# Optimization experiments

Hardware: AMD Instinct MI355X
Metric: run time of the kernel (lower is better)

Reference implementation:

```python
import jax, jax.numpy as jnp
import numpy as np

D_MODEL = 1024
HEAD_SIZE = 64
BLOCK_SIZE = 2048
B, T = 4, 2048


def setup_inputs() -> dict:
    key = jax.random.key(0)
    ks = jax.random.split(key, 7)
    s = 1.0 / np.sqrt(D_MODEL)
    x = jax.random.normal(ks[0], (B, T, D_MODEL), dtype=jnp.float32)
    Wq = jax.random.uniform(ks[1], (D_MODEL, HEAD_SIZE), jnp.float32, -s, s)
    bq = jax.random.uniform(ks[2], (HEAD_SIZE,), jnp.float32, -s, s)
    Wk = jax.random.uniform(ks[3], (D_MODEL, HEAD_SIZE), jnp.float32, -s, s)
    bk = jax.random.uniform(ks[4], (HEAD_SIZE,), jnp.float32, -s, s)
    Wv = jax.random.uniform(ks[5], (D_MODEL, HEAD_SIZE), jnp.float32, -s, s)
    return {"x": x, "Wq": Wq, "bq": bq, "Wk": Wk, "bk": bk, "Wv": Wv, "mask": 1}


def reference(x, Wq, bq, Wk, bk, Wv, mask):
    # x: [B, T, C]; single attention head, dropout is identity (eval/p=0)
    Tlen = x.shape[1]
    q = x @ Wq + bq              # [B, T, hs]
    k = x @ Wk + bk              # [B, T, hs]
    v = x @ Wv                   # [B, T, hs] (no bias)
    hs = k.shape[-1]
    # Faithful to source: weights = QK^T / hs**(-0.5)  ==  QK^T * sqrt(hs)
    w = jnp.einsum('btd,bsd->bts', q, k) * jnp.sqrt(jnp.asarray(hs, x.dtype))
    if mask:
        causal = jnp.tril(jnp.ones((Tlen, Tlen), dtype=bool))
        w = jnp.where(causal, w, jnp.asarray(-jnp.inf, w.dtype))
    w = jax.nn.softmax(w, axis=-1)
    out = jnp.einsum('bts,bsd->btd', w, v)  # [B, T, hs]
    return out
```

## Files before the change

kernel.cpp:

```cpp
#include <hip/hip_runtime.h>
#include <hip/hip_bf16.h>

#define D_MODEL 1024
#define HS 64
#define T_LEN 2048
#define JCH 256
#define NCH 8

typedef __attribute__((ext_vector_type(8))) short bf16x8;
typedef __attribute__((ext_vector_type(4))) float f32x4;

__device__ inline void split8(const float* v, int4& hi, int4& lo) {
    union { unsigned short u[8]; int4 v4; } uh, ul;
    #pragma unroll
    for (int i = 0; i < 8; ++i) {
        const unsigned int b = __float_as_uint(v[i]);
        const unsigned short h = (unsigned short)(b >> 16);
        const float r = v[i] - __uint_as_float((unsigned int)h << 16);
        uh.u[i] = h;
        ul.u[i] = (unsigned short)(__float_as_uint(r) >> 16);
    }
    hi = uh.v4; lo = ul.v4;
}

__device__ inline void split8b(const float* v, bf16x8& hi, bf16x8& lo) {
    union { unsigned short u[8]; bf16x8 v8; } uh, ul;
    #pragma unroll
    for (int i = 0; i < 8; ++i) {
        const unsigned int b = __float_as_uint(v[i]);
        const unsigned short h = (unsigned short)(b >> 16);
        const float r = v[i] - __uint_as_float((unsigned int)h << 16);
        uh.u[i] = h;
        ul.u[i] = (unsigned short)(__float_as_uint(r) >> 16);
    }
    hi = uh.v8; lo = ul.v8;
}

__device__ inline unsigned short f2bf_rne(float f) {
    const unsigned int b = __float_as_uint(f);
    return (unsigned short)((b + 0x7FFFu + ((b >> 16) & 1u)) >> 16);
}
__device__ inline float bf2f(unsigned short h) {
    return __uint_as_float((unsigned int)h << 16);
}

__device__ inline void async_copy16(const short* g, short* l) {
    __builtin_amdgcn_global_load_lds(
        (const __attribute__((address_space(1))) void*)g,
        (__attribute__((address_space(3))) void*)l, 16, 0, 0);
}

__global__ __launch_bounds__(256) void prep_kernel(
    const float* __restrict__ Wq, const float* __restrict__ Wk,
    const float* __restrict__ Wv,
    short* __restrict__ wh, short* __restrict__ wl)
{
    __shared__ float tile[64][69];
    const int tid = threadIdx.x;
    const int wb  = blockIdx.x;
    const int kb  = wb & 15;
    const int m   = wb >> 4;
    const float* W = (m == 0) ? Wq : (m == 1) ? Wk : Wv;
    #pragma unroll
    for (int it = 0; it < 4; ++it) {
        const int idx = tid + 256 * it;
        const int kr = idx >> 4, c4 = idx & 15;
        *(float4*)&tile[kr][4 * c4] =
            *(const float4*)(W + (size_t)(kb * 64 + kr) * HS + 4 * c4);
    }
    __syncthreads();
    #pragma unroll
    for (int i = 0; i < 2; ++i) {
        const int s    = tid + 256 * i;
        const int ntl  = s >> 7;
        const int kcl  = (s >> 6) & 1;
        const int lane = s & 63;
        const int n    = ntl * 16 + (lane & 15);
        const int krel = kcl * 32 + (lane >> 4) * 8;
        float v[8];
        #pragma unroll
        for (int e = 0; e < 8; ++e) v[e] = tile[krel + e][n];
        int4 hi, lo;
        split8(v, hi, lo);
        const size_t off =
            ((size_t)((m * 4 + ntl) * 32 + kb * 2 + kcl) * 64 + lane) * 8;
        *(int4*)(wh + off) = hi;
        *(int4*)(wl + off) = lo;
    }
}

__global__ __launch_bounds__(512, 2) void qkv_kernel(
    const float* __restrict__ x,
    const short* __restrict__ wh, const short* __restrict__ wl,
    const float* __restrict__ bq, const float* __restrict__ bk,
    short* __restrict__ qfh, short* __restrict__ qfl,
    short* __restrict__ kfh, short* __restrict__ kfl, short* __restrict__ vf)
{
    const int tid  = threadIdx.x;
    const int wv   = tid >> 6;
    const int lane = tid & 63;
    const int mt   = wv & 1;
    const int nt0  = (wv >> 1) * 3;
    const int r0   = blockIdx.x * 32;

    const float* xrow = x + (size_t)(r0 + mt * 16 + (lane & 15)) * D_MODEL
                          + (lane >> 4) * 8;

    f32x4 acc[3];
    #pragma unroll
    for (int j = 0; j < 3; ++j) acc[j] = (f32x4)(0.f);

    #pragma unroll
    for (int t = 0; t < 16; ++t) {
        const float* xc = xrow + t * 64;
        float v0[8], v1[8];
        *(float4*)&v0[0] = *(const float4*)(xc);
        *(float4*)&v0[4] = *(const float4*)(xc + 4);
        *(float4*)&v1[0] = *(const float4*)(xc + 32);
        *(float4*)&v1[4] = *(const float4*)(xc + 36);

        bf16x8 bh[2][3], bl[2][3];
        #pragma unroll
        for (int kcl = 0; kcl < 2; ++kcl)
            #pragma unroll
            for (int j = 0; j < 3; ++j) {
                const size_t off =
                    ((size_t)((nt0 + j) * 32 + t * 2 + kcl)) * 512 + lane * 8;
                bh[kcl][j] = *(const bf16x8*)&wh[off];
                bl[kcl][j] = *(const bf16x8*)&wl[off];
            }

        bf16x8 a0h, a0l, a1h, a1l;
        split8b(v0, a0h, a0l);
        split8b(v1, a1h, a1l);

        #pragma unroll
        for (int j = 0; j < 3; ++j) {
            acc[j] = __builtin_amdgcn_mfma_f32_16x16x32_bf16(a0h, bh[0][j], acc[j], 0, 0, 0);
            acc[j] = __builtin_amdgcn_mfma_f32_16x16x32_bf16(a0h, bl[0][j], acc[j], 0, 0, 0);
            acc[j] = __builtin_amdgcn_mfma_f32_16x16x32_bf16(a0l, bh[0][j], acc[j], 0, 0, 0);
        }
        #pragma unroll
        for (int j = 0; j < 3; ++j) {
            acc[j] = __builtin_amdgcn_mfma_f32_16x16x32_bf16(a1h, bh[1][j], acc[j], 0, 0, 0);
            acc[j] = __builtin_amdgcn_mfma_f32_16x16x32_bf16(a1h, bl[1][j], acc[j], 0, 0, 0);
            acc[j] = __builtin_amdgcn_mfma_f32_16x16x32_bf16(a1l, bh[1][j], acc[j], 0, 0, 0);
        }
    }

    const int quad = lane >> 4;
    const int l15  = lane & 15;
    const int rowb = r0 + mt * 16 + quad * 4;
    #pragma unroll
    for (int j = 0; j < 3; ++j) {
        const f32x4 a = acc[j];
        const int c = (nt0 + j) * 16 + l15;
        if (c < 128) {
            const int cc    = (c < 64) ? c : (c - 64);
            const float bias = (c < 64) ? bq[cc] : bk[cc];
            short* dsth = (c < 64) ? qfh : kfh;
            short* dstl = (c < 64) ? qfl : kfl;
            const int tile16 = rowb >> 4;
            const int kc2   = cc >> 5;
            const int quadd = (cc & 31) >> 3;
            const int e     = cc & 7;
            #pragma unroll
            for (int r = 0; r < 4; ++r) {
                const float val = a[r] + bias;
                const unsigned int b = __float_as_uint(val);
                const unsigned short h = (unsigned short)(b >> 16);
                const float res = val - __uint_as_float((unsigned int)h << 16);
                const unsigned short l16 = (unsigned short)(__float_as_uint(res) >> 16);
                const int laned = ((rowb + r) & 15) | (quadd << 4);
                const size_t off = ((size_t)((tile16 * 2 + kc2) * 64 + laned)) * 8 + e;
                dsth[off] = (short)h;
                dstl[off] = (short)l16;
            }
        } else {
            const int cv    = c - 128;
            const int vb    = rowb >> 6;
            const int jc2   = (rowb & 63) >> 5;
            const int quadd = (rowb & 31) >> 3;
            const int gg    = jc2 * 4 + (cv >> 4);
            const int laned = (cv & 15) | (quadd << 4);
            const size_t base = ((size_t)((vb * 8 + gg) * 64 + laned)) * 8 + (rowb & 7);
            short4 pk;
            pk.x = (short)f2bf_rne(a[0]);
            pk.y = (short)f2bf_rne(a[1]);
            pk.z = (short)f2bf_rne(a[2]);
            pk.w = (short)f2bf_rne(a[3]);
            *(short4*)(vf + base) = pk;
        }
    }
}

__global__ __launch_bounds__(256) void attn_kernel(
    const short* __restrict__ qfh, const short* __restrict__ qfl,
    const short* __restrict__ kfh, const short* __restrict__ kfl,
    const short* __restrict__ vf, const int* __restrict__ maskp,
    float* __restrict__ part_O, float* __restrict__ part_ml, int BT)
{
    __shared__ __align__(16) short Kh[4096], Kl[4096];
    __shared__ __align__(16) short Vt[4096];
    __shared__ __align__(16) short Pl[4][16 * 72];

    const int tile  = blockIdx.x;
    const int chunk = blockIdx.y;
    const int r0 = tile * 64;
    const int tb = r0 / T_LEN;
    const int t0 = r0 - tb * T_LEN;
    const int mask = (*maskp != 0);
    const int n_max = mask ? (t0 + 64) : T_LEN;
    const int j0 = chunk * JCH;
    if (j0 >= n_max) return;
    const int hi_j = min(j0 + JCH, n_max);
    const int njt = (hi_j - j0 + 63) >> 6;

    const int tid  = threadIdx.x;
    const int w    = tid >> 6;
    const int lane = tid & 63;
    const int quad = lane >> 4;
    const int l15  = lane & 15;
    const int rw0  = t0 + 16 * w;
    const int rowa = r0 + 16 * w + quad * 4;

    bf16x8 qh[2], ql[2];
    {
        const size_t qt = (size_t)(r0 >> 4) + w;
        #pragma unroll
        for (int kc = 0; kc < 2; ++kc) {
            qh[kc] = *(const bf16x8*)&qfh[((qt * 2 + kc) * 64 + lane) * 8];
            ql[kc] = *(const bf16x8*)&qfl[((qt * 2 + kc) * 64 + lane) * 8];
        }
    }

    f32x4 oacc[4];
    #pragma unroll
    for (int nt = 0; nt < 4; ++nt) oacc[nt] = (f32x4)(0.f);
    float m_r[4] = {-INFINITY, -INFINITY, -INFINITY, -INFINITY};
    float l_r[4] = {0.f, 0.f, 0.f, 0.f};

    for (int jt = 0; jt < njt; ++jt) {
        const int jbase = j0 + jt * 64;
        __syncthreads();
        {
            const size_t kt0 = (size_t)(tb * 128) + (jbase >> 4);
            const size_t vb  = (size_t)(tb * 32) + (jbase >> 6);
            #pragma unroll
            for (int ii = 0; ii < 6; ++ii) {
                const int g = w * 6 + ii;
                if (g < 8) {
                    const short* src = kfh + ((kt0 + (g >> 1)) * 2 + (g & 1)) * 512;
                    async_copy16(src + lane * 8, &Kh[g * 512]);
                } else if (g < 16) {
                    const int gg = g - 8;
                    const short* src = kfl + ((kt0 + (gg >> 1)) * 2 + (gg & 1)) * 512;
                    async_copy16(src + lane * 8, &Kl[gg * 512]);
                } else {
                    const int gg = g - 16;
                    const short* src = vf + (vb * 8 + gg) * 512;
                    async_copy16(src + lane * 8, &Vt[gg * 512]);
                }
            }
        }
        __syncthreads();

        const bool active = (!mask) || (jbase <= rw0 + 15);
        if (active) {
            f32x4 sacc[4];
            #pragma unroll
            for (int jsub = 0; jsub < 4; ++jsub) {
                f32x4 s = (f32x4)(0.f);
                #pragma unroll
                for (int kc = 0; kc < 2; ++kc) {
                    const bf16x8 kh = *(const bf16x8*)&Kh[((jsub * 2 + kc) * 64 + lane) * 8];
                    const bf16x8 kl = *(const bf16x8*)&Kl[((jsub * 2 + kc) * 64 + lane) * 8];
                    s = __builtin_amdgcn_mfma_f32_16x16x32_bf16(qh[kc], kh, s, 0, 0, 0);
                    s = __builtin_amdgcn_mfma_f32_16x16x32_bf16(qh[kc], kl, s, 0, 0, 0);
                    s = __builtin_amdgcn_mfma_f32_16x16x32_bf16(ql[kc], kh, s, 0, 0, 0);
                }
                sacc[jsub] = s;
            }
            float sval[4][4], rmax[4];
            #pragma unroll
            for (int r = 0; r < 4; ++r) rmax[r] = -INFINITY;
            #pragma unroll
            for (int jsub = 0; jsub < 4; ++jsub) {
                const int jg = jbase + jsub * 16 + l15;
                #pragma unroll
                for (int r = 0; r < 4; ++r) {
                    const int tg = rw0 + quad * 4 + r;
                    const float vv = (mask && (jg > tg)) ? -INFINITY : 8.0f * sacc[jsub][r];
                    sval[jsub][r] = vv;
                    rmax[r] = fmaxf(rmax[r], vv);
                }
            }
            #pragma unroll
            for (int d = 1; d < 16; d <<= 1)
                #pragma unroll
                for (int r = 0; r < 4; ++r)
                    rmax[r] = fmaxf(rmax[r], __shfl_xor(rmax[r], d));
            float alpha[4], msafe[4];
            #pragma unroll
            for (int r = 0; r < 4; ++r) {
                const float mn = fmaxf(m_r[r], rmax[r]);
                msafe[r] = (mn == -INFINITY) ? 0.f : mn;
                alpha[r] = __expf(m_r[r] - msafe[r]);
                m_r[r] = mn;
            }
            short* Pw = &Pl[w][0];
            float rsum[4] = {0.f, 0.f, 0.f, 0.f};
            #pragma unroll
            for (int jsub = 0; jsub < 4; ++jsub) {
                #pragma unroll
                for (int r = 0; r < 4; ++r) {
                    const float e = __expf(sval[jsub][r] - msafe[r]);
                    const unsigned short eb = f2bf_rne(e);
                    Pw[(quad * 4 + r) * 72 + jsub * 16 + l15] = (short)eb;
                    rsum[r] += bf2f(eb);
                }
            }
            #pragma unroll
            for (int d = 1; d < 16; d <<= 1)
                #pragma unroll
                for (int r = 0; r < 4; ++r)
                    rsum[r] += __shfl_xor(rsum[r], d);
            #pragma unroll
            for (int r = 0; r < 4; ++r)
                l_r[r] = l_r[r] * alpha[r] + rsum[r];
            #pragma unroll
            for (int nt = 0; nt < 4; ++nt)
                #pragma unroll
                for (int r = 0; r < 4; ++r)
                    oacc[nt][r] *= alpha[r];
            bf16x8 pf[2];
            #pragma unroll
            for (int jc = 0; jc < 2; ++jc)
                pf[jc] = *(const bf16x8*)&Pw[l15 * 72 + jc * 32 + quad * 8];
            #pragma unroll
            for (int nt = 0; nt < 4; ++nt) {
                #pragma unroll
                for (int jc = 0; jc < 2; ++jc) {
                    const bf16x8 vfr = *(const bf16x8*)&Vt[((jc * 4 + nt) * 64 + lane) * 8];
                    oacc[nt] = __builtin_amdgcn_mfma_f32_16x16x32_bf16(pf[jc], vfr, oacc[nt], 0, 0, 0);
                }
            }
        }
    }

    #pragma unroll
    for (int nt = 0; nt < 4; ++nt)
        #pragma unroll
        for (int r = 0; r < 4; ++r)
            part_O[((size_t)(rowa + r) * NCH + chunk) * HS + nt * 16 + l15] = oacc[nt][r];
    if (l15 == 0) {
        #pragma unroll
        for (int r = 0; r < 4; ++r) {
            float2 ml;
            ml.x = m_r[r];
            ml.y = l_r[r];
            *(float2*)(part_ml + ((size_t)(rowa + r) * NCH + chunk) * 2) = ml;
        }
    }
}

__global__ __launch_bounds__(256) void combine_kernel(
    const float* __restrict__ part_O, const float* __restrict__ part_ml,
    const int* __restrict__ maskp, float* __restrict__ out)
{
    const int f = blockIdx.x * 256 + threadIdx.x;
    const int row = f >> 4;
    const int d4 = (f & 15) * 4;
    const int t = row & (T_LEN - 1);
    const int mask = (*maskp != 0);
    const int n = mask ? (t + 1) : T_LEN;
    const int nc = (n + JCH - 1) / JCH;

    const float2* mlp = (const float2*)(part_ml + (size_t)row * NCH * 2);
    float M = -INFINITY;
    for (int c = 0; c < nc; ++c) M = fmaxf(M, mlp[c].x);
    float L = 0.f;
    float Ox = 0.f, Oy = 0.f, Oz = 0.f, Ow = 0.f;
    for (int c = 0; c < nc; ++c) {
        const float2 ml = mlp[c];
        const float w = __expf(ml.x - M);
        L += ml.y * w;
        const float4 p = *(const float4*)(part_O + ((size_t)row * NCH + c) * HS + d4);
        Ox = fmaf(p.x, w, Ox);
        Oy = fmaf(p.y, w, Oy);
        Oz = fmaf(p.z, w, Oz);
        Ow = fmaf(p.w, w, Ow);
    }
    float4 res;
    res.x = Ox / L;
    res.y = Oy / L;
    res.z = Oz / L;
    res.w = Ow / L;
    *(float4*)(out + (size_t)row * HS + d4) = res;
}

extern "C" void kernel_launch(void* const* d_in, const int* in_sizes, int n_in,
                              void* d_out, int out_size, void* d_ws, size_t ws_size,
                              hipStream_t stream) {
    const float* x  = (const float*)d_in[0];
    const float* Wq = (const float*)d_in[1];
    const float* bq = (const float*)d_in[2];
    const float* Wk = (const float*)d_in[3];
    const float* bk = (const float*)d_in[4];
    const float* Wv = (const float*)d_in[5];
    const int* maskp = (const int*)d_in[6];

    const int BT = in_sizes[0] / D_MODEL;

    float* pO  = (float*)d_ws;
    float* pml = pO + (size_t)BT * NCH * HS;
    short* wh  = (short*)(pml + (size_t)BT * NCH * 2);
    short* wl  = wh + (size_t)192 * D_MODEL;
    short* qfh = wl + (size_t)192 * D_MODEL;
    short* qfl = qfh + (size_t)BT * HS;
    short* kfh = qfl + (size_t)BT * HS;
    short* kfl = kfh + (size_t)BT * HS;
    short* vf  = kfl + (size_t)BT * HS;

    prep_kernel<<<48, 256, 0, stream>>>(Wq, Wk, Wv, wh, wl);
    qkv_kernel<<<BT / 32, 512, 0, stream>>>(x, wh, wl, bq, bk,
                                            qfh, qfl, kfh, kfl, vf);
    dim3 agrid(BT / 64, NCH);
    attn_kernel<<<agrid, 256, 0, stream>>>(qfh, qfl, kfh, kfl, vf, maskp,
                                           pO, pml, BT);
    combine_kernel<<<(BT * 16) / 256, 256, 0, stream>>>(pO, pml, maskp, (float*)d_out);
}
```

Before: 142.9 us.

## Split QKV projection into finer per-matrix blocks with XCD-aware block ordering

Result: slower. 165.1 us (+15.5%).

```diff
diff --git a/kernel.cpp b/kernel.cpp
--- a/kernel.cpp
+++ b/kernel.cpp
@@ -21,19 +21,6 @@
         ul.u[i] = (unsigned short)(__float_as_uint(r) >> 16);
     }
     hi = uh.v4; lo = ul.v4;
-}
-
-__device__ inline void split8b(const float* v, bf16x8& hi, bf16x8& lo) {
-    union { unsigned short u[8]; bf16x8 v8; } uh, ul;
-    #pragma unroll
-    for (int i = 0; i < 8; ++i) {
-        const unsigned int b = __float_as_uint(v[i]);
-        const unsigned short h = (unsigned short)(b >> 16);
-        const float r = v[i] - __uint_as_float((unsigned int)h << 16);
-        uh.u[i] = h;
-        ul.u[i] = (unsigned short)(__float_as_uint(r) >> 16);
-    }
-    hi = uh.v8; lo = ul.v8;
 }
 
 __device__ inline unsigned short f2bf_rne(float f) {
@@ -89,108 +76,108 @@
     }
 }
 
-__global__ __launch_bounds__(512, 2) void qkv_kernel(
+__device__ __forceinline__ void split_frag(const float4& p, const float4& q,
+                                           bf16x8& hi, bf16x8& lo) {
+    const float v[8] = {p.x, p.y, p.z, p.w, q.x, q.y, q.z, q.w};
+    #pragma unroll
+    for (int i = 0; i < 8; ++i) {
+        const unsigned int b = __float_as_uint(v[i]);
+        const unsigned short h = (unsigned short)(b >> 16);
+        const float r = v[i] - __uint_as_float((unsigned int)h << 16);
+        hi[i] = (short)h;
+        lo[i] = (short)(__float_as_uint(r) >> 16);
+    }
+}
+
+__global__ __launch_bounds__(256, 4) void qkv_kernel(
     const float* __restrict__ x,
     const short* __restrict__ wh, const short* __restrict__ wl,
     const float* __restrict__ bq, const float* __restrict__ bk,
     short* __restrict__ qfh, short* __restrict__ qfl,
-    short* __restrict__ kfh, short* __restrict__ kfl, short* __restrict__ vf)
+    short* __restrict__ kfh, short* __restrict__ kfl, short* __restrict__ vf,
+    int BT)
 {
     const int tid  = threadIdx.x;
-    const int wv   = tid >> 6;
+    const int w    = tid >> 6;
     const int lane = tid & 63;
-    const int mt   = wv & 1;
-    const int nt0  = (wv >> 1) * 3;
-    const int r0   = blockIdx.x * 32;
-
-    const float* xrow = x + (size_t)(r0 + mt * 16 + (lane & 15)) * D_MODEL
+
+    const int perx = ((BT >> 4) * 3) >> 3;
+    const int work = ((int)blockIdx.x >> 3) + ((int)blockIdx.x & 7) * perx;
+    const int g    = work / 3;
+    const int m    = work - g * 3;
+    const int r0   = g * 16;
+    const int gnt  = m * 4 + w;
+
+    const float* xrow = x + (size_t)(r0 + (lane & 15)) * D_MODEL
                           + (lane >> 4) * 8;
 
-    f32x4 acc[3];
-    #pragma unroll
-    for (int j = 0; j < 3; ++j) acc[j] = (f32x4)(0.f);
+    f32x4 acc = (f32x4)(0.f);
 
     #pragma unroll
     for (int t = 0; t < 16; ++t) {
+        const size_t ob0 = ((size_t)(gnt * 32 + t * 2 + 0)) * 512 + lane * 8;
+        const size_t ob1 = ((size_t)(gnt * 32 + t * 2 + 1)) * 512 + lane * 8;
+        const bf16x8 bh0 = *(const bf16x8*)&wh[ob0];
+        const bf16x8 bl0 = *(const bf16x8*)&wl[ob0];
+        const bf16x8 bh1 = *(const bf16x8*)&wh[ob1];
+        const bf16x8 bl1 = *(const bf16x8*)&wl[ob1];
+
         const float* xc = xrow + t * 64;
-        float v0[8], v1[8];
-        *(float4*)&v0[0] = *(const float4*)(xc);
-        *(float4*)&v0[4] = *(const float4*)(xc + 4);
-        *(float4*)&v1[0] = *(const float4*)(xc + 32);
-        *(float4*)&v1[4] = *(const float4*)(xc + 36);
-
-        bf16x8 bh[2][3], bl[2][3];
-        #pragma unroll
-        for (int kcl = 0; kcl < 2; ++kcl)
-            #pragma unroll
-            for (int j = 0; j < 3; ++j) {
-                const size_t off =
-                    ((size_t)((nt0 + j) * 32 + t * 2 + kcl)) * 512 + lane * 8;
-                bh[kcl][j] = *(const bf16x8*)&wh[off];
-                bl[kcl][j] = *(const bf16x8*)&wl[off];
-            }
+        const float4 xa = *(const float4*)(xc);
+        const float4 xb = *(const float4*)(xc + 4);
+        const float4 xm = *(const float4*)(xc + 32);
+        const float4 xd = *(const float4*)(xc + 36);
 
         bf16x8 a0h, a0l, a1h, a1l;
-        split8b(v0, a0h, a0l);
-        split8b(v1, a1h, a1l);
-
-        #pragma unroll
-        for (int j = 0; j < 3; ++j) {
-            acc[j] = __builtin_amdgcn_mfma_f32_16x16x32_bf16(a0h, bh[0][j], acc[j], 0, 0, 0);
-            acc[j] = __builtin_amdgcn_mfma_f32_16x16x32_bf16(a0h, bl[0][j], acc[j], 0, 0, 0);
-            acc[j] = __builtin_amdgcn_mfma_f32_16x16x32_bf16(a0l, bh[0][j], acc[j], 0, 0, 0);
-        }
-        #pragma unroll
-        for (int j = 0; j < 3; ++j) {
-            acc[j] = __builtin_amdgcn_mfma_f32_16x16x32_bf16(a1h, bh[1][j], acc[j], 0, 0, 0);
-            acc[j] = __builtin_amdgcn_mfma_f32_16x16x32_bf16(a1h, bl[1][j], acc[j], 0, 0, 0);
-            acc[j] = __builtin_amdgcn_mfma_f32_16x16x32_bf16(a1l, bh[1][j], acc[j], 0, 0, 0);
-        }
+        split_frag(xa, xb, a0h, a0l);
+        split_frag(xm, xd, a1h, a1l);
+
+        acc = __builtin_amdgcn_mfma_f32_16x16x32_bf16(a0h, bh0, acc, 0, 0, 0);
+        acc = __builtin_amdgcn_mfma_f32_16x16x32_bf16(a0h, bl0, acc, 0, 0, 0);
+        acc = __builtin_amdgcn_mfma_f32_16x16x32_bf16(a0l, bh0, acc, 0, 0, 0);
+        acc = __builtin_amdgcn_mfma_f32_16x16x32_bf16(a1h, bh1, acc, 0, 0, 0);
+        acc = __builtin_amdgcn_mfma_f32_16x16x32_bf16(a1h, bl1, acc, 0, 0, 0);
+        acc = __builtin_amdgcn_mfma_f32_16x16x32_bf16(a1l, bh1, acc, 0, 0, 0);
     }
 
     const int quad = lane >> 4;
     const int l15  = lane & 15;
-    const int rowb = r0 + mt * 16 + quad * 4;
-    #pragma unroll
-    for (int j = 0; j < 3; ++j) {
-        const f32x4 a = acc[j];
-        const int c = (nt0 + j) * 16 + l15;
-        if (c < 128) {
-            const int cc    = (c < 64) ? c : (c - 64);
-            const float bias = (c < 64) ? bq[cc] : bk[cc];
-            short* dsth = (c < 64) ? qfh : kfh;
-            short* dstl = (c < 64) ? qfl : kfl;
-            const int tile16 = rowb >> 4;
-            const int kc2   = cc >> 5;
-            const int quadd = (cc & 31) >> 3;
-            const int e     = cc & 7;
-            #pragma unroll
-            for (int r = 0; r < 4; ++r) {
-                const float val = a[r] + bias;
-                const unsigned int b = __float_as_uint(val);
-                const unsigned short h = (unsigned short)(b >> 16);
-                const float res = val - __uint_as_float((unsigned int)h << 16);
-                const unsigned short l16 = (unsigned short)(__float_as_uint(res) >> 16);
-                const int laned = ((rowb + r) & 15) | (quadd << 4);
-                const size_t off = ((size_t)((tile16 * 2 + kc2) * 64 + laned)) * 8 + e;
-                dsth[off] = (short)h;
-                dstl[off] = (short)l16;
-            }
-        } else {
-            const int cv    = c - 128;
-            const int vb    = rowb >> 6;
-            const int jc2   = (rowb & 63) >> 5;
-            const int quadd = (rowb & 31) >> 3;
-            const int gg    = jc2 * 4 + (cv >> 4);
-            const int laned = (cv & 15) | (quadd << 4);
-            const size_t base = ((size_t)((vb * 8 + gg) * 64 + laned)) * 8 + (rowb & 7);
-            short4 pk;
-            pk.x = (short)f2bf_rne(a[0]);
-            pk.y = (short)f2bf_rne(a[1]);
-            pk.z = (short)f2bf_rne(a[2]);
-            pk.w = (short)f2bf_rne(a[3]);
-            *(short4*)(vf + base) = pk;
+    const int rowb = r0 + quad * 4;
+    const int cc   = w * 16 + l15;
+    if (m < 2) {
+        const float bias = (m == 0) ? bq[cc] : bk[cc];
+        short* dsth = (m == 0) ? qfh : kfh;
+        short* dstl = (m == 0) ? qfl : kfl;
+        const int tile16 = rowb >> 4;
+        const int kc2   = cc >> 5;
+        const int quadd = (cc & 31) >> 3;
+        const int e     = cc & 7;
+        #pragma unroll
+        for (int r = 0; r < 4; ++r) {
+            const float val = acc[r] + bias;
+            const unsigned int b = __float_as_uint(val);
+            const unsigned short h = (unsigned short)(b >> 16);
+            const float res = val - __uint_as_float((unsigned int)h << 16);
+            const unsigned short l16 = (unsigned short)(__float_as_uint(res) >> 16);
+            const int laned = ((rowb + r) & 15) | (quadd << 4);
+            const size_t off = ((size_t)((tile16 * 2 + kc2) * 64 + laned)) * 8 + e;
+            dsth[off] = (short)h;
+            dstl[off] = (short)l16;
         }
+    } else {
+        const int cv    = cc;
+        const int vb    = rowb >> 6;
+        const int jc2   = (rowb & 63) >> 5;
+        const int quadd = (rowb & 31) >> 3;
+        const int gg    = jc2 * 4 + (cv >> 4);
+        const int laned = (cv & 15) | (quadd << 4);
+        const size_t base = ((size_t)((vb * 8 + gg) * 64 + laned)) * 8 + (rowb & 7);
+        short4 pk;
+        pk.x = (short)f2bf_rne(acc[0]);
+        pk.y = (short)f2bf_rne(acc[1]);
+        pk.z = (short)f2bf_rne(acc[2]);
+        pk.w = (short)f2bf_rne(acc[3]);
+        *(short4*)(vf + base) = pk;
     }
 }
 
@@ -423,8 +410,8 @@
     short* vf  = kfl + (size_t)BT * HS;
 
     prep_kernel<<<48, 256, 0, stream>>>(Wq, Wk, Wv, wh, wl);
-    qkv_kernel<<<BT / 32, 512, 0, stream>>>(x, wh, wl, bq, bk,
-                                            qfh, qfl, kfh, kfl, vf);
+    qkv_kernel<<<3 * (BT / 16), 256, 0, stream>>>(x, wh, wl, bq, bk,
+                                                  qfh, qfl, kfh, kfl, vf, BT);
     dim3 agrid(BT / 64, NCH);
     attn_kernel<<<agrid, 256, 0, stream>>>(qfh, qfl, kfh, kfl, vf, maskp,
                                            pO, pml, BT);
```
